# Optimization experiments

Hardware: AMD Instinct MI355X
Metric: run time of the kernel (lower is better)

## Reference

```python
import jax, jax.numpy as jnp
from jax import lax
import numpy as np

B, N, C = 512, 196, 384
H = 12
D = C // H
A = 49          # agent_num
W = 14          # window; N == W*W, pool 14x14 -> 7x7
SCALE = D ** -0.5


def setup_inputs() -> dict:
    key = jax.random.key(0)
    ks = jax.random.split(key, 12)
    f = lambda k, s, std=0.02: (jax.random.normal(k, s, dtype=jnp.float32) * std)
    return {
        "x": jax.random.normal(ks[0], (B, N, C), dtype=jnp.float32),
        "qkv_w": f(ks[1], (3 * C, C)),
        "proj_w": f(ks[2], (C, C)),
        "proj_b": jnp.zeros((C,), jnp.float32),
        "dwc_w": f(ks[3], (C, 1, 3, 3)),      # depthwise: groups == C
        "dwc_b": jnp.zeros((C,), jnp.float32),
        "an_bias": f(ks[4], (H, A, 7, 7)),
        "ah_bias": f(ks[5], (1, H, A, W, 1)),
        "aw_bias": f(ks[6], (1, H, A, 1, W)),
        "na_bias": f(ks[7], (H, A, 7, 7)),
        "ha_bias": f(ks[8], (1, H, W, 1, A)),
        "wa_bias": f(ks[9], (1, H, 1, W, A)),
    }


def reference(x, qkv_w, proj_w, proj_b, dwc_w, dwc_b,
              an_bias, ah_bias, aw_bias, na_bias, ha_bias, wa_bias):
    b, n, c = x.shape
    # qkv projection (no bias)
    qkv = x @ qkv_w.T                                   # (b, n, 3c)
    q, k, v = jnp.split(qkv, 3, axis=-1)                # each (b, n, c)

    # agent tokens: adaptive avg pool of q from 14x14 to 7x7 (exact 2x2 mean)
    agent = q.reshape(b, 7, 2, 7, 2, c).mean(axis=(2, 4)).reshape(b, A, c)

    qh = q.reshape(b, n, H, D).transpose(0, 2, 1, 3)    # (b, H, n, D)
    kh = k.reshape(b, n, H, D).transpose(0, 2, 1, 3)
    vh = v.reshape(b, n, H, D).transpose(0, 2, 1, 3)
    ag = agent.reshape(b, A, H, D).transpose(0, 2, 1, 3)  # (b, H, A, D)

    # agent->kv attention bias: bilinear upsample 7x7 -> 14x14 (align_corners=False)
    pb1 = jax.image.resize(an_bias, (H, A, W, W), method='bilinear').reshape(1, H, A, n)
    pb2 = (ah_bias + aw_bias).reshape(1, H, A, n)
    agent_attn = jax.nn.softmax(
        jnp.einsum('bhad,bhnd->bhan', ag * SCALE, kh) + pb1 + pb2, axis=-1)
    agent_v = jnp.einsum('bhan,bhnd->bhad', agent_attn, vh)   # (b, H, A, D)

    # query->agent attention bias
    ab1 = jax.image.resize(na_bias, (H, A, W, W), method='bilinear') \
            .reshape(1, H, A, n).transpose(0, 1, 3, 2)          # (1, H, n, A)
    ab2 = (ha_bias + wa_bias).reshape(1, H, n, A)
    q_attn = jax.nn.softmax(
        jnp.einsum('bhnd,bhad->bhna', qh * SCALE, ag) + ab1 + ab2, axis=-1)
    out = jnp.einsum('bhna,bhad->bhnd', q_attn, agent_v)        # (b, H, n, D)
    out = out.transpose(0, 2, 1, 3).reshape(b, n, c)

    # depthwise 3x3 conv over v (NCHW), residual add
    v_img = v.reshape(b, W, W, c).transpose(0, 3, 1, 2)         # (b, c, 14, 14)
    dwc = lax.conv_general_dilated(
        v_img, dwc_w, window_strides=(1, 1), padding=((1, 1), (1, 1)),
        dimension_numbers=('NCHW', 'OIHW', 'NCHW'), feature_group_count=c)
    dwc = dwc + dwc_b[None, :, None, None]
    out = out + dwc.transpose(0, 2, 3, 1).reshape(b, n, c)

    return out @ proj_w.T + proj_b
```

## Files before the change

### kernel.cpp

```cpp
#include <hip/hip_runtime.h>

typedef unsigned short u16;
typedef unsigned int   u32;

#define SCALE 0.17677669529663687f

using bf16x8 = __attribute__((ext_vector_type(8))) __bf16;
using f32x4  = __attribute__((ext_vector_type(4))) float;

__device__ __forceinline__ float bf2f(u16 u) {
  union { u32 i; float f; } c; c.i = ((u32)u) << 16; return c.f;
}
__device__ __forceinline__ u16 f2bf(float f) {
  union { float f; u32 i; } c; c.f = f;
  u32 x = c.i;
  return (u16)((x + 0x7fffu + ((x >> 16) & 1u)) >> 16);
}

__device__ __forceinline__ void gl_lds16(const void* g, void* l) {
  __builtin_amdgcn_global_load_lds(
      (__attribute__((address_space(1))) void*)(uintptr_t)g,
      (__attribute__((address_space(3))) void*)(uintptr_t)l, 16, 0, 0);
}

__device__ __forceinline__ bf16x8 lds8(const u16* p) {
  union { bf16x8 v; uint2 u[2]; } r;
  r.u[0] = *(const uint2*)p;
  r.u[1] = *(const uint2*)(p + 4);
  return r.v;
}

__device__ __forceinline__ void lin_w(int i, int& i0, int& i1, float& w0, float& w1) {
  if (i == 0)       { i0 = 0; i1 = 0; w0 = 1.f;  w1 = 0.f;  }
  else if (i == 13) { i0 = 6; i1 = 6; w0 = 1.f;  w1 = 0.f;  }
  else if (i & 1)   { int j = i >> 1; i0 = j;     i1 = j + 1; w0 = 0.75f; w1 = 0.25f; }
  else              { int j = i >> 1; i0 = j - 1; i1 = j;     w0 = 0.25f; w1 = 0.75f; }
}

__global__ void k_bias1(const float* __restrict__ an, const float* __restrict__ ah,
                        const float* __restrict__ aw, float* __restrict__ out) {
  int idx = blockIdx.x * 256 + threadIdx.x;
  if (idx >= 12 * 49 * 196) return;
  int n = idx % 196; int a = (idx / 196) % 49; int h = idx / (196 * 49);
  int y = n / 14, x = n % 14;
  int y0, y1, x0, x1; float wy0, wy1, wx0, wx1;
  lin_w(y, y0, y1, wy0, wy1); lin_w(x, x0, x1, wx0, wx1);
  const float* p = an + (h * 49 + a) * 49;
  float v = wy0 * (wx0 * p[y0 * 7 + x0] + wx1 * p[y0 * 7 + x1])
          + wy1 * (wx0 * p[y1 * 7 + x0] + wx1 * p[y1 * 7 + x1]);
  v += ah[(h * 49 + a) * 14 + y] + aw[(h * 49 + a) * 14 + x];
  out[idx] = v;
}

__global__ void k_bias2(const float* __restrict__ na, const float* __restrict__ ha,
                        const float* __restrict__ wa, float* __restrict__ out) {
  int idx = blockIdx.x * 256 + threadIdx.x;
  if (idx >= 12 * 196 * 49) return;
  int a = idx % 49; int n = (idx / 49) % 196; int h = idx / (49 * 196);
  int y = n / 14, x = n % 14;
  int y0, y1, x0, x1; float wy0, wy1, wx0, wx1;
  lin_w(y, y0, y1, wy0, wy1); lin_w(x, x0, x1, wx0, wx1);
  const float* p = na + (h * 49 + a) * 49;
  float v = wy0 * (wx0 * p[y0 * 7 + x0] + wx1 * p[y0 * 7 + x1])
          + wy1 * (wx0 * p[y1 * 7 + x0] + wx1 * p[y1 * 7 + x1]);
  v += ha[(h * 14 + y) * 49 + a] + wa[(h * 14 + x) * 49 + a];
  out[idx] = v;
}

__global__ void k_f2bf(const float* __restrict__ src, u16* __restrict__ dst, long n) {
  long i = ((long)blockIdx.x * 256 + threadIdx.x) * 8;
  if (i >= n) return;
  float4 a = *(const float4*)(src + i);
  float4 b = *(const float4*)(src + i + 4);
  union { u16 s[8]; uint4 v; } pk;
  pk.s[0] = f2bf(a.x); pk.s[1] = f2bf(a.y); pk.s[2] = f2bf(a.z); pk.s[3] = f2bf(a.w);
  pk.s[4] = f2bf(b.x); pk.s[5] = f2bf(b.y); pk.s[6] = f2bf(b.z); pk.s[7] = f2bf(b.w);
  *(uint4*)(dst + i) = pk.v;
}

__global__ __launch_bounds__(256) void k_mfma_qkv(const u16* __restrict__ A,
    const u16* __restrict__ Bw, u16* __restrict__ out) {
  __shared__ __align__(16) u16 As[128 * 64];
  __shared__ __align__(16) u16 Bs[128 * 64];
  const int tid = threadIdx.x;
  const int lane = tid & 63, w = tid >> 6;
  const int wm = (w >> 1) * 64, wn = (w & 1) * 64;
  const long row0 = (long)blockIdx.y * 128;
  const int col0 = blockIdx.x * 128;
  const int quad = lane >> 4, m16 = lane & 15;
  f32x4 acc[4][4] = {};
  for (int kt = 0; kt < 6; ++kt) {
    const int k0 = kt * 64;
    __syncthreads();
#pragma unroll
    for (int i = 0; i < 4; ++i) {
      int c = i * 256 + w * 64 + lane;
      const u16* ga = A + (row0 + (c >> 3)) * 384 + k0 + (c & 7) * 8;
      gl_lds16(ga, &As[(i * 256 + w * 64) * 8]);
      const u16* gb = Bw + (long)(col0 + (c >> 3)) * 384 + k0 + (c & 7) * 8;
      gl_lds16(gb, &Bs[(i * 256 + w * 64) * 8]);
    }
    __syncthreads();
#pragma unroll
    for (int kk = 0; kk < 2; ++kk) {
      bf16x8 av[4], bv[4];
#pragma unroll
      for (int i = 0; i < 4; ++i)
        av[i] = *(const bf16x8*)&As[(wm + i * 16 + m16) * 64 + kk * 32 + quad * 8];
#pragma unroll
      for (int j = 0; j < 4; ++j)
        bv[j] = *(const bf16x8*)&Bs[(wn + j * 16 + m16) * 64 + kk * 32 + quad * 8];
#pragma unroll
      for (int i = 0; i < 4; ++i)
#pragma unroll
        for (int j = 0; j < 4; ++j)
          acc[i][j] = __builtin_amdgcn_mfma_f32_16x16x32_bf16(av[i], bv[j], acc[i][j], 0, 0, 0);
    }
  }
#pragma unroll
  for (int i = 0; i < 4; ++i)
#pragma unroll
    for (int r = 0; r < 4; ++r) {
      long row = row0 + wm + i * 16 + quad * 4 + r;
      u16* op = out + row * 1152 + col0 + wn + m16;
#pragma unroll
      for (int j = 0; j < 4; ++j) op[j * 16] = f2bf(acc[i][j][r]);
    }
}

__global__ __launch_bounds__(256) void k_mfma_out(const u16* __restrict__ A,
    const u16* __restrict__ Bw, const float* __restrict__ pb, float* __restrict__ out) {
  __shared__ __align__(16) u16 As[128 * 64];
  __shared__ __align__(16) u16 Bs[128 * 64];
  const int tid = threadIdx.x;
  const int lane = tid & 63, w = tid >> 6;
  const int wm = (w >> 1) * 64, wn = (w & 1) * 64;
  const long row0 = (long)blockIdx.y * 128;
  const int col0 = blockIdx.x * 128;
  const int quad = lane >> 4, m16 = lane & 15;
  f32x4 acc[4][4] = {};
  for (int kt = 0; kt < 6; ++kt) {
    const int k0 = kt * 64;
    __syncthreads();
#pragma unroll
    for (int i = 0; i < 4; ++i) {
      int c = i * 256 + w * 64 + lane;
      const u16* ga = A + (row0 + (c >> 3)) * 384 + k0 + (c & 7) * 8;
      gl_lds16(ga, &As[(i * 256 + w * 64) * 8]);
      const u16* gb = Bw + (long)(col0 + (c >> 3)) * 384 + k0 + (c & 7) * 8;
      gl_lds16(gb, &Bs[(i * 256 + w * 64) * 8]);
    }
    __syncthreads();
#pragma unroll
    for (int kk = 0; kk < 2; ++kk) {
      bf16x8 av[4], bv[4];
#pragma unroll
      for (int i = 0; i < 4; ++i)
        av[i] = *(const bf16x8*)&As[(wm + i * 16 + m16) * 64 + kk * 32 + quad * 8];
#pragma unroll
      for (int j = 0; j < 4; ++j)
        bv[j] = *(const bf16x8*)&Bs[(wn + j * 16 + m16) * 64 + kk * 32 + quad * 8];
#pragma unroll
      for (int i = 0; i < 4; ++i)
#pragma unroll
        for (int j = 0; j < 4; ++j)
          acc[i][j] = __builtin_amdgcn_mfma_f32_16x16x32_bf16(av[i], bv[j], acc[i][j], 0, 0, 0);
    }
  }
  float pbv[4];
#pragma unroll
  for (int j = 0; j < 4; ++j) pbv[j] = pb[col0 + wn + j * 16 + m16];
#pragma unroll
  for (int i = 0; i < 4; ++i)
#pragma unroll
    for (int r = 0; r < 4; ++r) {
      long row = row0 + wm + i * 16 + quad * 4 + r;
      float* op = out + row * 384 + col0 + wn + m16;
#pragma unroll
      for (int j = 0; j < 4; ++j) op[j * 16] = acc[i][j][r] + pbv[j];
    }
}

#define OFF_SCR   0
#define OFF_DWCS  4608
#define OFF_AVT   17152
#define OFF_VS    21504
#define OFF_P2    21504
#define OFF_AGS   35616
#define OFF_DWCW  39144
#define SMEM_BYTES 39808

__global__ __launch_bounds__(256, 4) void k_fused(const u16* __restrict__ qkv,
    const float* __restrict__ bias1, const float* __restrict__ bias2,
    const float* __restrict__ dwc_w, const float* __restrict__ dwc_b,
    u16* __restrict__ t) {
  __shared__ __align__(16) char smem[SMEM_BYTES];
  u16* AVt  = (u16*)(smem + OFF_AVT);
  u16* dwcs = (u16*)(smem + OFF_DWCS);
  u16* Vs   = (u16*)(smem + OFF_VS);
  u16* ags  = (u16*)(smem + OFF_AGS);
  u16* dwcw = (u16*)(smem + OFF_DWCW);

  const int bh = blockIdx.x, b = bh / 12, h = bh % 12;
  const int tid = threadIdx.x;
  const int lane = tid & 63, w = tid >> 6;
  const int quad = lane >> 4, m16 = lane & 15;
  u16* scr = (u16*)(smem + OFF_SCR) + w * 576;
  u16* P2w = (u16*)(smem + OFF_P2)  + w * 1088;
  const long qkvb = (long)b * 196 * 1152;
  const f32x4 zf = {0.f, 0.f, 0.f, 0.f};

  if (tid < 196) {
    const uint2* v2p = (const uint2*)(qkv + qkvb + (long)tid * 1152 + 768 + h * 32);
    uint2* vd = (uint2*)&Vs[tid * 36];
#pragma unroll
    for (int i = 0; i < 8; ++i) vd[i] = v2p[i];
  }
  for (int i = tid; i < 320; i += 256) {
    int tap = i >> 5, ch = i & 31;
    float v = (tap < 9) ? dwc_w[(h * 32 + ch) * 9 + tap] : dwc_b[h * 32 + ch];
    dwcw[tap * 32 + ch] = f2bf(v);
  }
  for (int i = tid; i < 784; i += 256) {
    int a = i >> 4, cp = i & 15;
    int ay = a / 7, ax = a % 7;
    int y0 = ay * 2, x0 = ax * 2;
    const u16* q0 = qkv + qkvb + h * 32 + cp * 2;
    u32 v00 = *(const u32*)(q0 + (long)(y0 * 14 + x0) * 1152);
    u32 v01 = *(const u32*)(q0 + (long)(y0 * 14 + x0 + 1) * 1152);
    u32 v10 = *(const u32*)(q0 + (long)((y0 + 1) * 14 + x0) * 1152);
    u32 v11 = *(const u32*)(q0 + (long)((y0 + 1) * 14 + x0 + 1) * 1152);
    float lo = 0.25f * (bf2f((u16)(v00 & 0xffff)) + bf2f((u16)(v01 & 0xffff))
                      + bf2f((u16)(v10 & 0xffff)) + bf2f((u16)(v11 & 0xffff)));
    float hi = 0.25f * (bf2f((u16)(v00 >> 16)) + bf2f((u16)(v01 >> 16))
                      + bf2f((u16)(v10 >> 16)) + bf2f((u16)(v11 >> 16)));
    *(u32*)&ags[a * 36 + cp * 2] = (u32)f2bf(lo) | ((u32)f2bf(hi) << 16);
  }
  __syncthreads();

  {
    int ar = 16 * w + m16; if (ar > 48) ar = 48;
    bf16x8 av = lds8(&ags[ar * 36 + quad * 8]);
    const u16* kq = qkv + qkvb + 384 + h * 32 + quad * 8;
    const float* b1 = bias1 + (long)h * 49 * 196;
    f32x4 avacc[2] = {zf, zf};
    float rs[4] = {0.f, 0.f, 0.f, 0.f};
    for (int k7 = 0; k7 < 7; ++k7) {
#pragma unroll
      for (int t2 = 0; t2 < 2; ++t2) {
        int nt = k7 * 2 + t2;
        if (nt < 13) {
          int tk = nt * 16 + m16; if (tk > 195) tk = 195;
          bf16x8 bv = *(const bf16x8*)(kq + (long)tk * 1152);
          f32x4 s = __builtin_amdgcn_mfma_f32_16x16x32_bf16(av, bv, zf, 0, 0, 0);
#pragma unroll
          for (int r = 0; r < 4; ++r) {
            int agent = 16 * w + quad * 4 + r;
            int token = nt * 16 + m16;
            float e = 0.f;
            if (agent < 49 && token < 196)
              e = __expf(s[r] * SCALE + b1[agent * 196 + token]);
            rs[r] += e;
            scr[(quad * 4 + r) * 36 + t2 * 16 + m16] = f2bf(e);
          }
        } else {
#pragma unroll
          for (int r = 0; r < 4; ++r)
            scr[(quad * 4 + r) * 36 + t2 * 16 + m16] = 0;
        }
      }
      bf16x8 ap = lds8(&scr[m16 * 36 + quad * 8]);
#pragma unroll
      for (int ntc = 0; ntc < 2; ++ntc) {
        union { u16 s[8]; bf16x8 v; } bp;
#pragma unroll
        for (int j = 0; j < 8; ++j) {
          int tok = k7 * 32 + quad * 8 + j;
          bp.s[j] = (tok < 196) ? Vs[tok * 36 + ntc * 16 + m16] : (u16)0;
        }
        avacc[ntc] = __builtin_amdgcn_mfma_f32_16x16x32_bf16(ap, bp.v, avacc[ntc], 0, 0, 0);
      }
    }
    float inv[4];
#pragma unroll
    for (int r = 0; r < 4; ++r) {
      rs[r] += __shfl_xor(rs[r], 1);
      rs[r] += __shfl_xor(rs[r], 2);
      rs[r] += __shfl_xor(rs[r], 4);
      rs[r] += __shfl_xor(rs[r], 8);
      inv[r] = (16 * w + quad * 4 + r < 49) ? 1.f / rs[r] : 0.f;
    }
#pragma unroll
    for (int ntc = 0; ntc < 2; ++ntc)
#pragma unroll
      for (int r = 0; r < 4; ++r)
        AVt[(ntc * 16 + m16) * 68 + 16 * w + quad * 4 + r] = f2bf(avacc[ntc][r] * inv[r]);
  }

  {
    int cp = tid & 15, slot = tid >> 4;
    float wv[20];
#pragma unroll
    for (int tp = 0; tp < 10; ++tp) {
      u32 ww = *(const u32*)&dwcw[tp * 32 + cp * 2];
      wv[2 * tp] = bf2f((u16)(ww & 0xffff));
      wv[2 * tp + 1] = bf2f((u16)(ww >> 16));
    }
    for (int token = slot; token < 196; token += 16) {
      int y = token / 14, x = token % 14;
      float a0 = wv[18], a1 = wv[19];
      int tap = 0;
      for (int dy = -1; dy <= 1; ++dy) {
        int yy = y + dy;
        for (int dx = -1; dx <= 1; ++dx, ++tap) {
          int xx = x + dx;
          if (yy < 0 || yy > 13 || xx < 0 || xx > 13) continue;
          u32 vv = *(const u32*)&Vs[(yy * 14 + xx) * 36 + cp * 2];
          a0 += wv[2 * tap] * bf2f((u16)(vv & 0xffff));
          a1 += wv[2 * tap + 1] * bf2f((u16)(vv >> 16));
        }
      }
      *(u32*)&dwcs[token * 32 + cp * 2] = (u32)f2bf(a0) | ((u32)f2bf(a1) << 16);
    }
  }
  __syncthreads();

  const float* b2 = bias2 + (long)h * 196 * 49;
  for (int mt = w; mt < 13; mt += 4) {
    int tka = mt * 16 + m16; if (tka > 195) tka = 195;
    bf16x8 aq = *(const bf16x8*)(qkv + qkvb + (long)tka * 1152 + h * 32 + quad * 8);
    f32x4 sacc[4];
#pragma unroll
    for (int nt = 0; nt < 4; ++nt) {
      int gr = nt * 16 + m16; if (gr > 48) gr = 48;
      bf16x8 bv = lds8(&ags[gr * 36 + quad * 8]);
      sacc[nt] = __builtin_amdgcn_mfma_f32_16x16x32_bf16(aq, bv, zf, 0, 0, 0);
    }
    float rs[4] = {0.f, 0.f, 0.f, 0.f};
#pragma unroll
    for (int nt = 0; nt < 4; ++nt) {
      int agent = nt * 16 + m16;
#pragma unroll
      for (int r = 0; r < 4; ++r) {
        int token = mt * 16 + quad * 4 + r; if (token > 195) token = 195;
        float e = 0.f;
        if (agent < 49)
          e = __expf(sacc[nt][r] * SCALE + b2[token * 49 + agent]);
        sacc[nt][r] = e;
        rs[r] += e;
      }
    }
    float inv[4];
#pragma unroll
    for (int r = 0; r < 4; ++r) {
      rs[r] += __shfl_xor(rs[r], 1);
      rs[r] += __shfl_xor(rs[r], 2);
      rs[r] += __shfl_xor(rs[r], 4);
      rs[r] += __shfl_xor(rs[r], 8);
      inv[r] = 1.f / rs[r];
    }
#pragma unroll
    for (int nt = 0; nt < 4; ++nt)
#pragma unroll
      for (int r = 0; r < 4; ++r)
        P2w[(quad * 4 + r) * 68 + nt * 16 + m16] = f2bf(sacc[nt][r] * inv[r]);
    f32x4 oacc[2] = {zf, zf};
#pragma unroll
    for (int k2 = 0; k2 < 2; ++k2) {
      bf16x8 ap = lds8(&P2w[m16 * 68 + k2 * 32 + quad * 8]);
#pragma unroll
      for (int nt2 = 0; nt2 < 2; ++nt2) {
        bf16x8 bv = lds8(&AVt[(nt2 * 16 + m16) * 68 + k2 * 32 + quad * 8]);
        oacc[nt2] = __builtin_amdgcn_mfma_f32_16x16x32_bf16(ap, bv, oacc[nt2], 0, 0, 0);
      }
    }
#pragma unroll
    for (int nt2 = 0; nt2 < 2; ++nt2)
#pragma unroll
      for (int r = 0; r < 4; ++r) {
        int token = mt * 16 + quad * 4 + r;
        if (token < 196) {
          int ch = nt2 * 16 + m16;
          float val = oacc[nt2][r] + bf2f(dwcs[token * 32 + ch]);
          t[((long)(b * 196 + token)) * 384 + h * 32 + ch] = f2bf(val);
        }
      }
  }
}

extern "C" void kernel_launch(void* const* d_in, const int* in_sizes, int n_in,
                              void* d_out, int out_size, void* d_ws, size_t ws_size,
                              hipStream_t stream) {
  (void)in_sizes; (void)n_in; (void)out_size; (void)ws_size;
  const float* x      = (const float*)d_in[0];
  const float* qkv_w  = (const float*)d_in[1];
  const float* proj_w = (const float*)d_in[2];
  const float* proj_b = (const float*)d_in[3];
  const float* dwc_w  = (const float*)d_in[4];
  const float* dwc_b  = (const float*)d_in[5];
  const float* an_b   = (const float*)d_in[6];
  const float* ah_b   = (const float*)d_in[7];
  const float* aw_b   = (const float*)d_in[8];
  const float* na_b   = (const float*)d_in[9];
  const float* ha_b   = (const float*)d_in[10];
  const float* wa_b   = (const float*)d_in[11];
  float* out = (float*)d_out;

  char* ws = (char*)d_ws;
  u16*   qkv     = (u16*)ws;
  u16*   t       = (u16*)(ws + 231211008);
  u16*   xb      = (u16*)(ws + 308281344);
  u16*   wqkvb   = (u16*)(ws + 385351680);
  u16*   wprojb  = (u16*)(ws + 386236416);
  float* bias1   = (float*)(ws + 386531328);
  float* bias2   = (float*)(ws + 386992320);

  k_bias1<<<451, 256, 0, stream>>>(an_b, ah_b, aw_b, bias1);
  k_bias2<<<451, 256, 0, stream>>>(na_b, ha_b, wa_b, bias2);
  k_f2bf<<<18816, 256, 0, stream>>>(x, xb, (long)100352 * 384);
  k_f2bf<<<216, 256, 0, stream>>>(qkv_w, wqkvb, (long)1152 * 384);
  k_f2bf<<<72, 256, 0, stream>>>(proj_w, wprojb, (long)384 * 384);
  k_mfma_qkv<<<dim3(9, 784), 256, 0, stream>>>(xb, wqkvb, qkv);
  k_fused<<<6144, 256, 0, stream>>>(qkv, bias1, bias2, dwc_w, dwc_b, t);
  k_mfma_out<<<dim3(3, 784), 256, 0, stream>>>(t, wprojb, proj_b, out);
}
```

Before: 800.1 us.

## Transpose V in LDS, store biases as bf16, and remap blocks per XCD

```diff
diff --git a/kernel.cpp b/kernel.cpp
--- a/kernel.cpp
+++ b/kernel.cpp
@@ -38,25 +38,29 @@
 }
 
 __global__ void k_bias1(const float* __restrict__ an, const float* __restrict__ ah,
-                        const float* __restrict__ aw, float* __restrict__ out) {
+                        const float* __restrict__ aw, u16* __restrict__ out) {
+  int idx = blockIdx.x * 256 + threadIdx.x;
+  if (idx >= 12 * 196 * 52) return;
+  int a = idx % 52; int n = (idx / 52) % 196; int h = idx / (52 * 196);
+  u16 res = 0;
+  if (a < 49) {
+    int y = n / 14, x = n % 14;
+    int y0, y1, x0, x1; float wy0, wy1, wx0, wx1;
+    lin_w(y, y0, y1, wy0, wy1); lin_w(x, x0, x1, wx0, wx1);
+    const float* p = an + (h * 49 + a) * 49;
+    float v = wy0 * (wx0 * p[y0 * 7 + x0] + wx1 * p[y0 * 7 + x1])
+            + wy1 * (wx0 * p[y1 * 7 + x0] + wx1 * p[y1 * 7 + x1]);
+    v += ah[(h * 49 + a) * 14 + y] + aw[(h * 49 + a) * 14 + x];
+    res = f2bf(v);
+  }
+  out[idx] = res;
+}
+
+__global__ void k_bias2(const float* __restrict__ na, const float* __restrict__ ha,
+                        const float* __restrict__ wa, u16* __restrict__ out) {
   int idx = blockIdx.x * 256 + threadIdx.x;
   if (idx >= 12 * 49 * 196) return;
   int n = idx % 196; int a = (idx / 196) % 49; int h = idx / (196 * 49);
-  int y = n / 14, x = n % 14;
-  int y0, y1, x0, x1; float wy0, wy1, wx0, wx1;
-  lin_w(y, y0, y1, wy0, wy1); lin_w(x, x0, x1, wx0, wx1);
-  const float* p = an + (h * 49 + a) * 49;
-  float v = wy0 * (wx0 * p[y0 * 7 + x0] + wx1 * p[y0 * 7 + x1])
-          + wy1 * (wx0 * p[y1 * 7 + x0] + wx1 * p[y1 * 7 + x1]);
-  v += ah[(h * 49 + a) * 14 + y] + aw[(h * 49 + a) * 14 + x];
-  out[idx] = v;
-}
-
-__global__ void k_bias2(const float* __restrict__ na, const float* __restrict__ ha,
-                        const float* __restrict__ wa, float* __restrict__ out) {
-  int idx = blockIdx.x * 256 + threadIdx.x;
-  if (idx >= 12 * 196 * 49) return;
-  int a = idx % 49; int n = (idx / 49) % 196; int h = idx / (49 * 196);
   int y = n / 14, x = n % 14;
   int y0, y1, x0, x1; float wy0, wy1, wx0, wx1;
   lin_w(y, y0, y1, wy0, wy1); lin_w(x, x0, x1, wx0, wx1);
@@ -64,7 +68,7 @@
   float v = wy0 * (wx0 * p[y0 * 7 + x0] + wx1 * p[y0 * 7 + x1])
           + wy1 * (wx0 * p[y1 * 7 + x0] + wx1 * p[y1 * 7 + x1]);
   v += ha[(h * 14 + y) * 49 + a] + wa[(h * 14 + x) * 49 + a];
-  out[idx] = v;
+  out[idx] = f2bf(v);
 }
 
 __global__ void k_f2bf(const float* __restrict__ src, u16* __restrict__ dst, long n) {
@@ -82,11 +86,13 @@
     const u16* __restrict__ Bw, u16* __restrict__ out) {
   __shared__ __align__(16) u16 As[128 * 64];
   __shared__ __align__(16) u16 Bs[128 * 64];
+  const int orig = blockIdx.x;
+  const int wg = (orig & 7) * 882 + (orig >> 3);
+  const long row0 = (long)(wg / 9) * 128;
+  const int col0 = (wg % 9) * 128;
   const int tid = threadIdx.x;
   const int lane = tid & 63, w = tid >> 6;
   const int wm = (w >> 1) * 64, wn = (w & 1) * 64;
-  const long row0 = (long)blockIdx.y * 128;
-  const int col0 = blockIdx.x * 128;
   const int quad = lane >> 4, m16 = lane & 15;
   f32x4 acc[4][4] = {};
   for (int kt = 0; kt < 6; ++kt) {
@@ -132,11 +138,13 @@
     const u16* __restrict__ Bw, const float* __restrict__ pb, float* __restrict__ out) {
   __shared__ __align__(16) u16 As[128 * 64];
   __shared__ __align__(16) u16 Bs[128 * 64];
+  const int orig = blockIdx.x;
+  const int wg = (orig & 7) * 294 + (orig >> 3);
+  const long row0 = (long)(wg / 3) * 128;
+  const int col0 = (wg % 3) * 128;
   const int tid = threadIdx.x;
   const int lane = tid & 63, w = tid >> 6;
   const int wm = (w >> 1) * 64, wn = (w & 1) * 64;
-  const long row0 = (long)blockIdx.y * 128;
-  const int col0 = blockIdx.x * 128;
   const int quad = lane >> 4, m16 = lane & 15;
   f32x4 acc[4][4] = {};
   for (int kt = 0; kt < 6; ++kt) {
@@ -184,24 +192,27 @@
 #define OFF_SCR   0
 #define OFF_DWCS  4608
 #define OFF_AVT   17152
-#define OFF_VS    21504
+#define OFF_VT    21504
 #define OFF_P2    21504
-#define OFF_AGS   35616
-#define OFF_DWCW  39144
-#define SMEM_BYTES 39808
+#define OFF_AGS   34560
+#define OFF_DWCW  38088
+#define SMEM_BYTES 38784
+#define VT_PITCH  204
 
 __global__ __launch_bounds__(256, 4) void k_fused(const u16* __restrict__ qkv,
-    const float* __restrict__ bias1, const float* __restrict__ bias2,
+    const u16* __restrict__ b1t, const u16* __restrict__ b2t,
     const float* __restrict__ dwc_w, const float* __restrict__ dwc_b,
     u16* __restrict__ t) {
   __shared__ __align__(16) char smem[SMEM_BYTES];
   u16* AVt  = (u16*)(smem + OFF_AVT);
   u16* dwcs = (u16*)(smem + OFF_DWCS);
-  u16* Vs   = (u16*)(smem + OFF_VS);
+  u16* Vt   = (u16*)(smem + OFF_VT);
   u16* ags  = (u16*)(smem + OFF_AGS);
   u16* dwcw = (u16*)(smem + OFF_DWCW);
 
-  const int bh = blockIdx.x, b = bh / 12, h = bh % 12;
+  const int orig = blockIdx.x;
+  const int bh = (orig & 7) * 768 + (orig >> 3);
+  const int b = bh / 12, h = bh % 12;
   const int tid = threadIdx.x;
   const int lane = tid & 63, w = tid >> 6;
   const int quad = lane >> 4, m16 = lane & 15;
@@ -212,10 +223,16 @@
 
   if (tid < 196) {
     const uint2* v2p = (const uint2*)(qkv + qkvb + (long)tid * 1152 + 768 + h * 32);
-    uint2* vd = (uint2*)&Vs[tid * 36];
-#pragma unroll
-    for (int i = 0; i < 8; ++i) vd[i] = v2p[i];
-  }
+    u32 vv[16];
+#pragma unroll
+    for (int i = 0; i < 8; ++i) { uint2 d = v2p[i]; vv[2 * i] = d.x; vv[2 * i + 1] = d.y; }
+#pragma unroll
+    for (int i = 0; i < 16; ++i) {
+      Vt[(2 * i) * VT_PITCH + tid]     = (u16)(vv[i] & 0xffff);
+      Vt[(2 * i + 1) * VT_PITCH + tid] = (u16)(vv[i] >> 16);
+    }
+  }
+  { int ch = tid >> 3, tk = 196 + (tid & 7); Vt[ch * VT_PITCH + tk] = 0; }
   for (int i = tid; i < 320; i += 256) {
     int tap = i >> 5, ch = i & 31;
     float v = (tap < 9) ? dwc_w[(h * 32 + ch) * 9 + tap] : dwc_b[h * 32 + ch];
@@ -242,7 +259,7 @@
     int ar = 16 * w + m16; if (ar > 48) ar = 48;
     bf16x8 av = lds8(&ags[ar * 36 + quad * 8]);
     const u16* kq = qkv + qkvb + 384 + h * 32 + quad * 8;
-    const float* b1 = bias1 + (long)h * 49 * 196;
+    const u16* b1 = b1t + (long)h * 196 * 52;
     f32x4 avacc[2] = {zf, zf};
     float rs[4] = {0.f, 0.f, 0.f, 0.f};
     for (int k7 = 0; k7 < 7; ++k7) {
@@ -250,16 +267,18 @@
       for (int t2 = 0; t2 < 2; ++t2) {
         int nt = k7 * 2 + t2;
         if (nt < 13) {
-          int tk = nt * 16 + m16; if (tk > 195) tk = 195;
+          int token = nt * 16 + m16;
+          int tk = token; if (tk > 195) tk = 195;
           bf16x8 bv = *(const bf16x8*)(kq + (long)tk * 1152);
           f32x4 s = __builtin_amdgcn_mfma_f32_16x16x32_bf16(av, bv, zf, 0, 0, 0);
+          union { uint2 v; u16 s4[4]; } bb;
+          bb.v = *(const uint2*)(b1 + token * 52 + 16 * w + quad * 4);
 #pragma unroll
           for (int r = 0; r < 4; ++r) {
             int agent = 16 * w + quad * 4 + r;
-            int token = nt * 16 + m16;
             float e = 0.f;
             if (agent < 49 && token < 196)
-              e = __expf(s[r] * SCALE + b1[agent * 196 + token]);
+              e = __expf(s[r] * SCALE + bf2f(bb.s4[r]));
             rs[r] += e;
             scr[(quad * 4 + r) * 36 + t2 * 16 + m16] = f2bf(e);
           }
@@ -272,13 +291,8 @@
       bf16x8 ap = lds8(&scr[m16 * 36 + quad * 8]);
 #pragma unroll
       for (int ntc = 0; ntc < 2; ++ntc) {
-        union { u16 s[8]; bf16x8 v; } bp;
-#pragma unroll
-        for (int j = 0; j < 8; ++j) {
-          int tok = k7 * 32 + quad * 8 + j;
-          bp.s[j] = (tok < 196) ? Vs[tok * 36 + ntc * 16 + m16] : (u16)0;
-        }
-        avacc[ntc] = __builtin_amdgcn_mfma_f32_16x16x32_bf16(ap, bp.v, avacc[ntc], 0, 0, 0);
+        bf16x8 bvv = lds8(&Vt[(ntc * 16 + m16) * VT_PITCH + k7 * 32 + quad * 8]);
+        avacc[ntc] = __builtin_amdgcn_mfma_f32_16x16x32_bf16(ap, bvv, avacc[ntc], 0, 0, 0);
       }
     }
     float inv[4];
@@ -298,34 +312,36 @@
   }
 
   {
-    int cp = tid & 15, slot = tid >> 4;
-    float wv[20];
-#pragma unroll
-    for (int tp = 0; tp < 10; ++tp) {
-      u32 ww = *(const u32*)&dwcw[tp * 32 + cp * 2];
-      wv[2 * tp] = bf2f((u16)(ww & 0xffff));
-      wv[2 * tp + 1] = bf2f((u16)(ww >> 16));
-    }
-    for (int token = slot; token < 196; token += 16) {
-      int y = token / 14, x = token % 14;
-      float a0 = wv[18], a1 = wv[19];
-      int tap = 0;
+    int ch = tid & 31, slot = tid >> 5;
+    const u16* Vr = &Vt[ch * VT_PITCH];
+    float wv[10];
+#pragma unroll
+    for (int tp = 0; tp < 10; ++tp) wv[tp] = bf2f(dwcw[tp * 32 + ch]);
+    for (int p = slot; p < 98; p += 8) {
+      int t0 = 2 * p;
+      int y = t0 / 14, x0 = t0 % 14;
+      float a0 = wv[9], a1 = wv[9];
+#pragma unroll
       for (int dy = -1; dy <= 1; ++dy) {
         int yy = y + dy;
-        for (int dx = -1; dx <= 1; ++dx, ++tap) {
-          int xx = x + dx;
-          if (yy < 0 || yy > 13 || xx < 0 || xx > 13) continue;
-          u32 vv = *(const u32*)&Vs[(yy * 14 + xx) * 36 + cp * 2];
-          a0 += wv[2 * tap] * bf2f((u16)(vv & 0xffff));
-          a1 += wv[2 * tap + 1] * bf2f((u16)(vv >> 16));
-        }
-      }
-      *(u32*)&dwcs[token * 32 + cp * 2] = (u32)f2bf(a0) | ((u32)f2bf(a1) << 16);
+        if (yy < 0 || yy > 13) continue;
+        int tb = yy * 14 + x0;
+        float wl = wv[(dy + 1) * 3], wc = wv[(dy + 1) * 3 + 1], wr = wv[(dy + 1) * 3 + 2];
+        u32 vm = *(const u32*)(Vr + tb);
+        float vx0 = bf2f((u16)(vm & 0xffff)), vx1 = bf2f((u16)(vm >> 16));
+        float vxm1 = 0.f, vx2 = 0.f;
+        if (x0 > 0)  { u32 vl = *(const u32*)(Vr + tb - 2); vxm1 = bf2f((u16)(vl >> 16)); }
+        if (x0 < 12) { u32 vr2 = *(const u32*)(Vr + tb + 2); vx2 = bf2f((u16)(vr2 & 0xffff)); }
+        a0 += wl * vxm1 + wc * vx0 + wr * vx1;
+        a1 += wl * vx0  + wc * vx1 + wr * vx2;
+      }
+      dwcs[t0 * 32 + ch]       = f2bf(a0);
+      dwcs[(t0 + 1) * 32 + ch] = f2bf(a1);
     }
   }
   __syncthreads();
 
-  const float* b2 = bias2 + (long)h * 196 * 49;
+  const u16* b2 = b2t + (long)h * 49 * 196;
   for (int mt = w; mt < 13; mt += 4) {
     int tka = mt * 16 + m16; if (tka > 195) tka = 195;
     bf16x8 aq = *(const bf16x8*)(qkv + qkvb + (long)tka * 1152 + h * 32 + quad * 8);
@@ -336,16 +352,18 @@
       bf16x8 bv = lds8(&ags[gr * 36 + quad * 8]);
       sacc[nt] = __builtin_amdgcn_mfma_f32_16x16x32_bf16(aq, bv, zf, 0, 0, 0);
     }
+    int tb = mt * 16 + quad * 4; if (tb > 192) tb = 192;
     float rs[4] = {0.f, 0.f, 0.f, 0.f};
 #pragma unroll
     for (int nt = 0; nt < 4; ++nt) {
       int agent = nt * 16 + m16;
+      union { uint2 v; u16 s4[4]; } bb;
+      bb.v = *(const uint2*)(b2 + agent * 196 + tb);
 #pragma unroll
       for (int r = 0; r < 4; ++r) {
-        int token = mt * 16 + quad * 4 + r; if (token > 195) token = 195;
         float e = 0.f;
         if (agent < 49)
-          e = __expf(sacc[nt][r] * SCALE + b2[token * 49 + agent]);
+          e = __expf(sacc[nt][r] * SCALE + bf2f(bb.s4[r]));
         sacc[nt][r] = e;
         rs[r] += e;
       }
@@ -412,15 +430,15 @@
   u16*   xb      = (u16*)(ws + 308281344);
   u16*   wqkvb   = (u16*)(ws + 385351680);
   u16*   wprojb  = (u16*)(ws + 386236416);
-  float* bias1   = (float*)(ws + 386531328);
-  float* bias2   = (float*)(ws + 386992320);
-
-  k_bias1<<<451, 256, 0, stream>>>(an_b, ah_b, aw_b, bias1);
-  k_bias2<<<451, 256, 0, stream>>>(na_b, ha_b, wa_b, bias2);
+  u16*   b1t     = (u16*)(ws + 386531328);
+  u16*   b2t     = (u16*)(ws + 386777344);
+
+  k_bias1<<<478, 256, 0, stream>>>(an_b, ah_b, aw_b, b1t);
+  k_bias2<<<451, 256, 0, stream>>>(na_b, ha_b, wa_b, b2t);
   k_f2bf<<<18816, 256, 0, stream>>>(x, xb, (long)100352 * 384);
   k_f2bf<<<216, 256, 0, stream>>>(qkv_w, wqkvb, (long)1152 * 384);
   k_f2bf<<<72, 256, 0, stream>>>(proj_w, wprojb, (long)384 * 384);
-  k_mfma_qkv<<<dim3(9, 784), 256, 0, stream>>>(xb, wqkvb, qkv);
-  k_fused<<<6144, 256, 0, stream>>>(qkv, bias1, bias2, dwc_w, dwc_b, t);
-  k_mfma_out<<<dim3(3, 784), 256, 0, stream>>>(t, wprojb, proj_b, out);
-}
+  k_mfma_qkv<<<7056, 256, 0, stream>>>(xb, wqkvb, qkv);
+  k_fused<<<6144, 256, 0, stream>>>(qkv, b1t, b2t, dwc_w, dwc_b, t);
+  k_mfma_out<<<2352, 256, 0, stream>>>(t, wprojb, proj_b, out);
+}
```

Result: faster. 728.5 us (-8.9%).
